# Optimization experiments

Measured on AMD Instinct MI355X. Metric: run time of the kernel, lower is better.

The kernel has to match this reference:

```python
import jax, jax.numpy as jnp
import numpy as np

LN_EPS = 1e-5


def _ln(h, g, b):
    mu = h.mean(-1, keepdims=True)
    var = ((h - mu) ** 2).mean(-1, keepdims=True)
    return (h - mu) / jnp.sqrt(var + LN_EPS) * g + b


def setup_inputs() -> dict:
    key = jax.random.key(0)
    ks = jax.random.split(key, 12)
    B, T, Cin, C, D, M = 16, 1024, 512, 1024, 256, 1024
    s = 0.02
    inp = {
        "x": jax.random.normal(ks[0], (B, T, Cin), jnp.float32),
        "masks": jnp.ones((B, T), jnp.float32),
        "W1": jax.random.normal(ks[1], (Cin, C), jnp.float32) * s,
        "g1": jnp.ones((C,), jnp.float32), "b1": jnp.zeros((C,), jnp.float32),
        "W2": jax.random.normal(ks[2], (C, C), jnp.float32) * s,
        "g2": jnp.ones((C,), jnp.float32), "b2": jnp.zeros((C,), jnp.float32),
        "W3": jax.random.normal(ks[3], (C, C), jnp.float32) * s,
        "g3": jnp.ones((C,), jnp.float32), "b3": jnp.zeros((C,), jnp.float32),
        "W4": jax.random.normal(ks[4], (C, C), jnp.float32) * s,
        "g4": jnp.ones((C,), jnp.float32), "b4": jnp.zeros((C,), jnp.float32),
        "W5": jax.random.normal(ks[5], (C, D), jnp.float32) * s,
        "b5": jnp.zeros((D,), jnp.float32),
        # Dirichlet(alpha=100) rows, as in the torch init: rows live on the simplex
        "embedding": jax.random.dirichlet(ks[6], jnp.full((D,), 100.0, jnp.float32), (M,)).astype(jnp.float32),
    }
    return inp


def reference(x, masks, W1, g1, b1, W2, g2, b2, W3, g3, b3, W4, g4, b4, W5, b5, embedding):
    h = jax.nn.relu(_ln(x @ W1, g1, b1))
    h = jax.nn.relu(_ln(h @ W2, g2, b2))
    h = jax.nn.relu(_ln(h @ W3, g3, b3))
    h = jax.nn.relu(_ln(h @ W4, g4, b4))
    z = h @ W5 + b5                              # [B, T, D]
    p = jax.nn.log_softmax(z, axis=-1)           # log-prob features

    B, T, D = p.shape
    p_flat = jax.lax.stop_gradient(p.reshape(-1, D))   # x.detach() in torch
    ep = jnp.exp(p_flat)                               # [N, D]
    # KL(exp(p) || e_m) summed over D, for all codes m:
    #   sum_d exp(p)*(p - log(e_m)) = rowsum(exp(p)*p) - exp(p) @ log(E)^T
    div = (ep * p_flat).sum(-1, keepdims=True) - ep @ jnp.log(embedding).T  # [N, M]
    idx = jnp.argmin(div, axis=-1)                     # [N]
    quant = jax.lax.stop_gradient(embedding[idx].reshape(B, T, D))

    # commitment loss: masked KL(exp(p) || quant.detach())
    kl = (jnp.exp(p) * (p - jnp.log(quant))).sum(-1)   # [B, T]
    loss = 0.25 * (kl * masks).mean(0).sum()

    # straight-through estimator
    q = p + jax.lax.stop_gradient(quant - p)
    return z, q, loss
```

## Files before the change

kernel.cpp:

```cpp
#include <hip/hip_runtime.h>
#include <hip/hip_bf16.h>
#include <stdint.h>

typedef __attribute__((ext_vector_type(4))) float f32x4;
typedef __attribute__((ext_vector_type(8))) __bf16 bf16x8;
typedef __attribute__((ext_vector_type(4))) __bf16 bf16x4;

#define LN_EPS 1e-5f

__device__ __forceinline__ void gload_lds16(const void* g, void* l) {
  __builtin_amdgcn_global_load_lds(
      (__attribute__((address_space(1))) void*)(uintptr_t)g,
      (__attribute__((address_space(3))) void*)(uint32_t)(uintptr_t)l,
      16, 0, 0);
}

__device__ __forceinline__ f32x4 mfma16(bf16x8 a, bf16x8 b, f32x4 c) {
  return __builtin_amdgcn_mfma_f32_16x16x32_bf16(a, b, c, 0, 0, 0);
}

__global__ __launch_bounds__(256) void k_cvt_bf16(const float* __restrict__ x,
                                                  __bf16* __restrict__ o) {
  int i = (blockIdx.x * 256 + threadIdx.x) * 8;
  f32x4 a = *(const f32x4*)(x + i);
  f32x4 b = *(const f32x4*)(x + i + 4);
  bf16x8 v;
#pragma unroll
  for (int j = 0; j < 4; ++j) { v[j] = (__bf16)a[j]; v[j + 4] = (__bf16)b[j]; }
  *(bf16x8*)(o + i) = v;
}

__global__ void k_transpose(const float* __restrict__ W, __bf16* __restrict__ Wt,
                            int K, int N) {
  __shared__ float t[32][33];
  int nt = blockIdx.x * 32, kt = blockIdx.y * 32;
  int tx = threadIdx.x, ty = threadIdx.y;
  t[ty][tx] = W[(size_t)(kt + ty) * N + nt + tx];
  __syncthreads();
  Wt[(size_t)(nt + ty) * K + kt + tx] = (__bf16)t[tx][ty];
}

__global__ void k_transpose3(const float* __restrict__ Wa, const float* __restrict__ Wb,
                             const float* __restrict__ Wc, __bf16* __restrict__ Ta,
                             __bf16* __restrict__ Tb, __bf16* __restrict__ Tc) {
  __shared__ float t[32][33];
  const float* W = blockIdx.z == 0 ? Wa : (blockIdx.z == 1 ? Wb : Wc);
  __bf16* T = blockIdx.z == 0 ? Ta : (blockIdx.z == 1 ? Tb : Tc);
  int nt = blockIdx.x * 32, kt = blockIdx.y * 32;
  int tx = threadIdx.x, ty = threadIdx.y;
  t[ty][tx] = W[(size_t)(kt + ty) * 1024 + nt + tx];
  __syncthreads();
  T[(size_t)(nt + ty) * 1024 + kt + tx] = (__bf16)t[tx][ty];
}

__global__ __launch_bounds__(256) void k_logE(const float* __restrict__ e,
                                              __bf16* __restrict__ o) {
  int i = blockIdx.x * 256 + threadIdx.x;
  o[i] = (__bf16)logf(e[i] * 256.0f);
}

__global__ __launch_bounds__(512, 2) void k_gemm256(
    const __bf16* __restrict__ A, const __bf16* __restrict__ Bt,
    __bf16* __restrict__ O, int N, int K) {
  __shared__ char lds[131072];
  const int tid = threadIdx.x;
  const int lane = tid & 63;
  const int wid = tid >> 6;
  const int wm = wid >> 2;
  const int wn = wid & 3;
  const int bm0 = blockIdx.x * 256;
  const int bn0 = blockIdx.y * 256;
  const int NT = K >> 6;

  const int slin = tid * 16;
  const int lrow = slin >> 7;
  const int scol = (slin & 127) ^ ((lrow & 7) << 4);
  const char* Ab = (const char*)A;
  const char* Bb = (const char*)Bt;
  const uint32_t rs = (uint32_t)K * 2;

  const int klo = (lane >> 4) * 16;
  const int sw = (lane & 7) << 4;
  const uint32_t kx0 = (uint32_t)(klo ^ sw);
  const uint32_t kx1 = (uint32_t)((64 + klo) ^ sw);
  const uint32_t abase = (uint32_t)(wm * 128 + (lane & 15)) * 128;
  const uint32_t bbase = (uint32_t)(wn * 64 + (lane & 15)) * 128;

  f32x4 acc[8][4];
#pragma unroll
  for (int i = 0; i < 8; ++i)
#pragma unroll
    for (int j = 0; j < 4; ++j) acc[i][j] = 0.0f;

#define LDSA(buf) (lds + (buf)*32768)
#define LDSB(buf) (lds + 65536 + (buf)*32768)
#define STAGE_A(t, h)                                                              \
  {                                                                                \
    const char* src = Ab + (size_t)(bm0 + (h)*128 + lrow) * rs + ((t) << 7) + scol;\
    char* dst = LDSA((t)&1) + (h)*16384 + slin;                                    \
    gload_lds16(src, dst);                                                         \
    gload_lds16(src + (size_t)64 * rs, dst + 8192);                                \
  }
#define STAGE_B(t, h)                                                              \
  {                                                                                \
    const char* src = Bb + (size_t)(bn0 + (h)*128 + lrow) * rs + ((t) << 7) + scol;\
    char* dst = LDSB((t)&1) + (h)*16384 + slin;                                    \
    gload_lds16(src, dst);                                                         \
    gload_lds16(src + (size_t)64 * rs, dst + 8192);                                \
  }

  STAGE_A(0, 0); STAGE_A(0, 1); STAGE_B(0, 0); STAGE_B(0, 1);
  STAGE_B(1, 0); STAGE_B(1, 1);
  asm volatile("s_waitcnt vmcnt(4)");
  __builtin_amdgcn_s_barrier();
  __builtin_amdgcn_sched_barrier(0);

  for (int t = 0; t < NT; ++t) {
    const char* Acur = LDSA(t & 1);
    const char* Bcur = LDSB(t & 1);

    if (t + 1 < NT) { STAGE_A(t + 1, 0); STAGE_A(t + 1, 1); }
    bf16x8 bF[4][2];
#pragma unroll
    for (int ni = 0; ni < 4; ++ni) {
      bF[ni][0] = *(const bf16x8*)(Bcur + bbase + ni * 2048 + kx0);
      bF[ni][1] = *(const bf16x8*)(Bcur + bbase + ni * 2048 + kx1);
    }
    {
      bf16x8 aF[4][2];
#pragma unroll
      for (int mi = 0; mi < 4; ++mi) {
        aF[mi][0] = *(const bf16x8*)(Acur + abase + mi * 2048 + kx0);
        aF[mi][1] = *(const bf16x8*)(Acur + abase + mi * 2048 + kx1);
      }
      __builtin_amdgcn_s_setprio(1);
#pragma unroll
      for (int mi = 0; mi < 4; ++mi)
#pragma unroll
        for (int ni = 0; ni < 4; ++ni) {
          acc[mi][ni] = mfma16(aF[mi][0], bF[ni][0], acc[mi][ni]);
          acc[mi][ni] = mfma16(aF[mi][1], bF[ni][1], acc[mi][ni]);
        }
      __builtin_amdgcn_s_setprio(0);
    }
    __builtin_amdgcn_s_barrier();
    __builtin_amdgcn_sched_barrier(0);

    if (t + 2 < NT) { STAGE_B(t + 2, 0); STAGE_B(t + 2, 1); }
    {
      bf16x8 aF[4][2];
#pragma unroll
      for (int mi = 0; mi < 4; ++mi) {
        aF[mi][0] = *(const bf16x8*)(Acur + abase + (mi + 4) * 2048 + kx0);
        aF[mi][1] = *(const bf16x8*)(Acur + abase + (mi + 4) * 2048 + kx1);
      }
      __builtin_amdgcn_s_setprio(1);
#pragma unroll
      for (int mi = 0; mi < 4; ++mi)
#pragma unroll
        for (int ni = 0; ni < 4; ++ni) {
          acc[mi + 4][ni] = mfma16(aF[mi][0], bF[ni][0], acc[mi + 4][ni]);
          acc[mi + 4][ni] = mfma16(aF[mi][1], bF[ni][1], acc[mi + 4][ni]);
        }
      __builtin_amdgcn_s_setprio(0);
    }
    if (t + 1 < NT) {
      asm volatile("s_waitcnt vmcnt(4)");
      __builtin_amdgcn_s_barrier();
      __builtin_amdgcn_sched_barrier(0);
    }
  }
#undef STAGE_A
#undef STAGE_B
#undef LDSA
#undef LDSB

  const int r0 = (lane >> 4) * 4;
  const int cc = lane & 15;
#pragma unroll
  for (int mi = 0; mi < 8; ++mi) {
#pragma unroll
    for (int ni = 0; ni < 4; ++ni) {
      int r = bm0 + wm * 128 + mi * 16 + r0;
      int c = bn0 + wn * 64 + ni * 16 + cc;
#pragma unroll
      for (int j = 0; j < 4; ++j)
        O[(size_t)(r + j) * N + c] = (__bf16)acc[mi][ni][j];
    }
  }
}

__global__ __launch_bounds__(256) void k_ln_relu(__bf16* __restrict__ h,
                                                 const float* __restrict__ g,
                                                 const float* __restrict__ b) {
  int lane = threadIdx.x & 63;
  int row = blockIdx.x * 4 + (threadIdx.x >> 6);
  __bf16* rp = h + (size_t)row * 1024;
  bf16x8 v0 = *(const bf16x8*)(rp + lane * 8);
  bf16x8 v1 = *(const bf16x8*)(rp + 512 + lane * 8);
  float f0[8], f1[8];
  float s = 0.f, sq = 0.f;
#pragma unroll
  for (int j = 0; j < 8; ++j) {
    f0[j] = (float)v0[j]; f1[j] = (float)v1[j];
    s += f0[j] + f1[j];
    sq += f0[j] * f0[j] + f1[j] * f1[j];
  }
#pragma unroll
  for (int d = 1; d < 64; d <<= 1) { s += __shfl_xor(s, d); sq += __shfl_xor(sq, d); }
  float mu = s * (1.0f / 1024.0f);
  float var = sq * (1.0f / 1024.0f) - mu * mu;
  float rstd = rsqrtf(var + LN_EPS);
  const f32x4* gv = (const f32x4*)g;
  const f32x4* bv = (const f32x4*)b;
  f32x4 ga0 = gv[lane * 2], ga1 = gv[lane * 2 + 1];
  f32x4 gb0 = gv[128 + lane * 2], gb1 = gv[128 + lane * 2 + 1];
  f32x4 ba0 = bv[lane * 2], ba1 = bv[lane * 2 + 1];
  f32x4 bb0 = bv[128 + lane * 2], bb1 = bv[128 + lane * 2 + 1];
  bf16x8 o0, o1;
#pragma unroll
  for (int j = 0; j < 4; ++j) {
    float t0 = (f0[j] - mu) * rstd * ga0[j] + ba0[j];
    float t1 = (f0[j + 4] - mu) * rstd * ga1[j] + ba1[j];
    float t2 = (f1[j] - mu) * rstd * gb0[j] + bb0[j];
    float t3 = (f1[j + 4] - mu) * rstd * gb1[j] + bb1[j];
    o0[j] = (__bf16)fmaxf(t0, 0.f);
    o0[j + 4] = (__bf16)fmaxf(t1, 0.f);
    o1[j] = (__bf16)fmaxf(t2, 0.f);
    o1[j + 4] = (__bf16)fmaxf(t3, 0.f);
  }
  *(bf16x8*)(rp + lane * 8) = o0;
  *(bf16x8*)(rp + 512 + lane * 8) = o1;
}

__global__ __launch_bounds__(256) void k_gemm_sm(
    const __bf16* __restrict__ A, const __bf16* __restrict__ Bt,
    const float* __restrict__ bias, float* __restrict__ z,
    __bf16* __restrict__ ep, float* __restrict__ sm) {
  const int K = 1024;
  __shared__ char lds[40960];
  char* ldsA = lds;
  char* ldsB = lds + 8192;
  const int tid = threadIdx.x;
  const int lane = tid & 63;
  const int wn = tid >> 6;
  const int bm0 = blockIdx.x * 64;
  const char* Ab = (const char*)A;
  const char* Bb = (const char*)Bt;
  const uint32_t rs = (uint32_t)K * 2;

  const int cc = lane & 15;
  uint32_t ra[2][4], rb[2][4];
  {
    const int sww = (lane & 7) << 4;
    const int gk = lane & 48;
#pragma unroll
    for (int kk = 0; kk < 2; ++kk) {
#pragma unroll
      for (int i = 0; i < 4; ++i) {
        uint32_t kb = (uint32_t)((kk * 64 + gk) ^ sww);
        ra[kk][i] = (uint32_t)(i * 16 + cc) * 128 + kb;
        rb[kk][i] = (uint32_t)(wn * 64 + i * 16 + cc) * 128 + kb;
      }
    }
  }

  f32x4 acc[4][4];
#pragma unroll
  for (int i = 0; i < 4; ++i)
#pragma unroll
    for (int j = 0; j < 4; ++j) acc[i][j] = 0.0f;

  for (int k0 = 0; k0 < K; k0 += 64) {
    __syncthreads();
#pragma unroll
    for (int i = 0; i < 2; ++i) {
      int lin = i * 4096 + tid * 16;
      int row = lin >> 7;
      int col = (lin & 127) ^ ((row & 7) << 4);
      gload_lds16(Ab + (size_t)(bm0 + row) * rs + k0 * 2 + col, ldsA + lin);
    }
#pragma unroll
    for (int i = 0; i < 8; ++i) {
      int lin = i * 4096 + tid * 16;
      int row = lin >> 7;
      int col = (lin & 127) ^ ((row & 7) << 4);
      gload_lds16(Bb + (size_t)row * rs + k0 * 2 + col, ldsB + lin);
    }
    __syncthreads();
#pragma unroll
    for (int kk = 0; kk < 2; ++kk) {
      bf16x8 af[4], bfv[4];
#pragma unroll
      for (int i = 0; i < 4; ++i) af[i] = *(const bf16x8*)(ldsA + ra[kk][i]);
#pragma unroll
      for (int i = 0; i < 4; ++i) bfv[i] = *(const bf16x8*)(ldsB + rb[kk][i]);
#pragma unroll
      for (int mi = 0; mi < 4; ++mi)
#pragma unroll
        for (int ni = 0; ni < 4; ++ni)
          acc[mi][ni] = mfma16(af[mi], bfv[ni], acc[mi][ni]);
    }
  }

  __syncthreads();
  float* stm = (float*)lds;
  float* sts = (float*)(lds + 1024);
  float* rowm = (float*)(lds + 2048);
  float* rows_ = (float*)(lds + 2304);

  const int r0 = (lane >> 4) * 4;
  float bvv[4];
#pragma unroll
  for (int ni = 0; ni < 4; ++ni) bvv[ni] = bias[wn * 64 + ni * 16 + cc];

#pragma unroll
  for (int mi = 0; mi < 4; ++mi) {
#pragma unroll
    for (int j = 0; j < 4; ++j) {
      float m = -3.4e38f;
#pragma unroll
      for (int ni = 0; ni < 4; ++ni) m = fmaxf(m, acc[mi][ni][j] + bvv[ni]);
#pragma unroll
      for (int d = 1; d < 16; d <<= 1) m = fmaxf(m, __shfl_xor(m, d));
      if (cc == 0) stm[wn * 64 + mi * 16 + r0 + j] = m;
    }
  }
  __syncthreads();
  if (tid < 64) {
    float m = fmaxf(fmaxf(stm[tid], stm[64 + tid]), fmaxf(stm[128 + tid], stm[192 + tid]));
    rowm[tid] = m;
  }
  __syncthreads();
#pragma unroll
  for (int mi = 0; mi < 4; ++mi) {
#pragma unroll
    for (int j = 0; j < 4; ++j) {
      int r = mi * 16 + r0 + j;
      float m = rowm[r];
      float s = 0.f;
#pragma unroll
      for (int ni = 0; ni < 4; ++ni) s += expf(acc[mi][ni][j] + bvv[ni] - m);
#pragma unroll
      for (int d = 1; d < 16; d <<= 1) s += __shfl_xor(s, d);
      if (cc == 0) sts[wn * 64 + r] = s;
    }
  }
  __syncthreads();
  if (tid < 64) {
    float s = sts[tid] + sts[64 + tid] + sts[128 + tid] + sts[192 + tid];
    rows_[tid] = s;
    sm[bm0 + tid] = rowm[tid] + logf(s);
  }
  __syncthreads();
#pragma unroll
  for (int mi = 0; mi < 4; ++mi) {
#pragma unroll
    for (int j = 0; j < 4; ++j) {
      int r = mi * 16 + r0 + j;
      float m = rowm[r];
      float inv = 1.0f / rows_[r];
      float* zp = z + (size_t)(bm0 + r) * 256;
      __bf16* epp = ep + (size_t)(bm0 + r) * 256;
#pragma unroll
      for (int ni = 0; ni < 4; ++ni) {
        int c = wn * 64 + ni * 16 + cc;
        float zz = acc[mi][ni][j] + bvv[ni];
        zp[c] = zz;
        epp[c] = (__bf16)(expf(zz - m) * inv);
      }
    }
  }
}

__global__ __launch_bounds__(256) void k_gemm_div(
    const __bf16* __restrict__ A, const __bf16* __restrict__ Bt,
    float* __restrict__ part_val, int* __restrict__ part_idx, int N, int K) {
  __shared__ char lds[32768];
  char* ldsA = lds;
  char* ldsB = lds + 16384;
  const int tid = threadIdx.x;
  const int lane = tid & 63;
  const int wid = tid >> 6;
  const int wm = wid >> 1, wn = wid & 1;
  const int bm0 = blockIdx.x * 128;
  const int bn0 = blockIdx.y * 128;

  const int slin = tid * 16;
  const int srow = slin >> 7;
  const int scol = (slin & 127) ^ ((srow & 7) << 4);

  const char* Ab = (const char*)A;
  const char* Bb = (const char*)Bt;
  const uint32_t rs = (uint32_t)K * 2;

  uint32_t ra[2][4], rb[2][4];
  {
    const int sw = (lane & 7) << 4;
    const int gk = lane & 48;
#pragma unroll
    for (int kk = 0; kk < 2; ++kk) {
#pragma unroll
      for (int i = 0; i < 4; ++i) {
        uint32_t kb = (uint32_t)((kk * 64 + gk) ^ sw);
        ra[kk][i] = (uint32_t)(wm * 64 + i * 16 + (lane & 15)) * 128 + kb;
        rb[kk][i] = (uint32_t)(wn * 64 + i * 16 + (lane & 15)) * 128 + kb;
      }
    }
  }

  f32x4 acc[4][4];
#pragma unroll
  for (int i = 0; i < 4; ++i)
#pragma unroll
    for (int j = 0; j < 4; ++j) acc[i][j] = 0.0f;

  for (int k0 = 0; k0 < K; k0 += 64) {
    __syncthreads();
    const uint32_t kbyte = (uint32_t)k0 * 2 + (uint32_t)scol;
#pragma unroll
    for (int i = 0; i < 4; ++i) {
      int row = i * 32 + srow;
      gload_lds16(Ab + (size_t)(bm0 + row) * rs + kbyte, ldsA + i * 4096 + slin);
    }
#pragma unroll
    for (int i = 0; i < 4; ++i) {
      int row = i * 32 + srow;
      gload_lds16(Bb + (size_t)(bn0 + row) * rs + kbyte, ldsB + i * 4096 + slin);
    }
    __syncthreads();
#pragma unroll
    for (int kk = 0; kk < 2; ++kk) {
      bf16x8 af[4], bfv[4];
#pragma unroll
      for (int i = 0; i < 4; ++i) af[i] = *(const bf16x8*)(ldsA + ra[kk][i]);
#pragma unroll
      for (int i = 0; i < 4; ++i) bfv[i] = *(const bf16x8*)(ldsB + rb[kk][i]);
#pragma unroll
      for (int mi = 0; mi < 4; ++mi)
#pragma unroll
        for (int ni = 0; ni < 4; ++ni)
          acc[mi][ni] = mfma16(af[mi], bfv[ni], acc[mi][ni]);
    }
  }

  const int r0 = (lane >> 4) * 4;
  const int cc = lane & 15;
  const int nch = N >> 6;
#pragma unroll
  for (int mi = 0; mi < 4; ++mi) {
#pragma unroll
    for (int j = 0; j < 4; ++j) {
      float v = acc[mi][0][j];
      int c = cc;
#pragma unroll
      for (int ni = 1; ni < 4; ++ni) {
        float v2 = acc[mi][ni][j];
        int c2 = ni * 16 + cc;
        if (v2 > v) { v = v2; c = c2; }
      }
#pragma unroll
      for (int d = 1; d < 16; d <<= 1) {
        float ov = __shfl_xor(v, d);
        int oc = __shfl_xor(c, d);
        if (ov > v || (ov == v && oc < c)) { v = ov; c = oc; }
      }
      if (cc == 0) {
        int r = bm0 + wm * 64 + mi * 16 + r0 + j;
        int chunk = (bn0 >> 6) + wn;
        part_val[r * nch + chunk] = v;
        part_idx[r * nch + chunk] = bn0 + wn * 64 + c;
      }
    }
  }
}

__global__ __launch_bounds__(256) void k_final(
    const float* __restrict__ part_val, const int* __restrict__ part_idx,
    const float* __restrict__ z, const float* __restrict__ sm,
    const float* __restrict__ emb, const float* __restrict__ masks,
    float* __restrict__ q, float* __restrict__ blockloss) {
  __shared__ float ls[4];
  int lane = threadIdx.x & 63;
  int w = threadIdx.x >> 6;
  int row = blockIdx.x * 4 + w;
  float v = -3.4e38f;
  int c = 0x7fffffff;
  if (lane < 16) { v = part_val[row * 16 + lane]; c = part_idx[row * 16 + lane]; }
#pragma unroll
  for (int d = 1; d < 16; d <<= 1) {
    float ov = __shfl_xor(v, d);
    int oc = __shfl_xor(c, d);
    if (ov > v || (ov == v && oc < c)) { v = ov; c = oc; }
  }
  int code = __shfl(c, 0);
  f32x4 ev = ((const f32x4*)(emb + (size_t)code * 256))[lane];
  ((f32x4*)(q + (size_t)row * 256))[lane] = ev;
  f32x4 zv = ((const f32x4*)(z + (size_t)row * 256))[lane];
  float smr = sm[row];
  float kl = 0.f;
#pragma unroll
  for (int j = 0; j < 4; ++j) {
    float pj = zv[j] - smr;
    kl += expf(pj) * (pj - logf(ev[j]));
  }
#pragma unroll
  for (int d = 1; d < 64; d <<= 1) kl += __shfl_xor(kl, d);
  if (lane == 0) ls[w] = kl * masks[row];
  __syncthreads();
  if (threadIdx.x == 0) blockloss[blockIdx.x] = ls[0] + ls[1] + ls[2] + ls[3];
}

__global__ __launch_bounds__(256) void k_loss_reduce(const float* __restrict__ bl,
                                                     float* __restrict__ out) {
  __shared__ float s[256];
  float a = 0.f;
#pragma unroll
  for (int i = 0; i < 16; ++i) a += bl[threadIdx.x + i * 256];
  s[threadIdx.x] = a;
  __syncthreads();
  for (int st = 128; st > 0; st >>= 1) {
    if (threadIdx.x < st) s[threadIdx.x] += s[threadIdx.x + st];
    __syncthreads();
  }
  if (threadIdx.x == 0) out[0] = s[0] * (0.25f / 16.0f);
}

extern "C" void kernel_launch(void* const* d_in, const int* in_sizes, int n_in,
                              void* d_out, int out_size, void* d_ws, size_t ws_size,
                              hipStream_t stream) {
  const float* x = (const float*)d_in[0];
  const float* masks = (const float*)d_in[1];
  const float* W1 = (const float*)d_in[2];
  const float* g1 = (const float*)d_in[3];
  const float* b1 = (const float*)d_in[4];
  const float* W2 = (const float*)d_in[5];
  const float* g2 = (const float*)d_in[6];
  const float* b2 = (const float*)d_in[7];
  const float* W3 = (const float*)d_in[8];
  const float* g3 = (const float*)d_in[9];
  const float* b3 = (const float*)d_in[10];
  const float* W4 = (const float*)d_in[11];
  const float* g4 = (const float*)d_in[12];
  const float* b4 = (const float*)d_in[13];
  const float* W5 = (const float*)d_in[14];
  const float* b5 = (const float*)d_in[15];
  const float* emb = (const float*)d_in[16];

  const int M = 16384;
  char* ws = (char*)d_ws;
  __bf16* bufA = (__bf16*)(ws);
  __bf16* bufB = (__bf16*)(ws + (32ull << 20));
  __bf16* W1t = (__bf16*)(ws + (64ull << 20));
  __bf16* W2t = (__bf16*)(ws + (65ull << 20));
  __bf16* W3t = (__bf16*)(ws + (67ull << 20));
  __bf16* W4t = (__bf16*)(ws + (69ull << 20));
  __bf16* W5t = (__bf16*)(ws + (71ull << 20));
  __bf16* logE = (__bf16*)(ws + (72ull << 20));
  float* part_val = (float*)(ws + (73ull << 20));
  int* part_idx = (int*)(ws + (74ull << 20));
  float* blockloss = (float*)(ws + (75ull << 20));
  float* sm = (float*)(ws + (76ull << 20));
  __bf16* ep = (__bf16*)(ws + (16ull << 20));

  float* z = (float*)d_out;
  float* q = z + (size_t)M * 256;
  float* lossp = z + 2ull * M * 256;

  dim3 tb32(32, 32);
  k_cvt_bf16<<<4096, 256, 0, stream>>>(x, bufB);
  k_transpose<<<dim3(32, 16), tb32, 0, stream>>>(W1, W1t, 512, 1024);
  k_transpose3<<<dim3(32, 32, 3), tb32, 0, stream>>>(W2, W3, W4, W2t, W3t, W4t);
  k_transpose<<<dim3(8, 32), tb32, 0, stream>>>(W5, W5t, 1024, 256);
  k_logE<<<1024, 256, 0, stream>>>(emb, logE);

  k_gemm256<<<dim3(64, 4), 512, 0, stream>>>(bufB, W1t, bufA, 1024, 512);
  k_ln_relu<<<4096, 256, 0, stream>>>(bufA, g1, b1);
  k_gemm256<<<dim3(64, 4), 512, 0, stream>>>(bufA, W2t, bufB, 1024, 1024);
  k_ln_relu<<<4096, 256, 0, stream>>>(bufB, g2, b2);
  k_gemm256<<<dim3(64, 4), 512, 0, stream>>>(bufB, W3t, bufA, 1024, 1024);
  k_ln_relu<<<4096, 256, 0, stream>>>(bufA, g3, b3);
  k_gemm256<<<dim3(64, 4), 512, 0, stream>>>(bufA, W4t, bufB, 1024, 1024);
  k_ln_relu<<<4096, 256, 0, stream>>>(bufB, g4, b4);
  k_gemm_sm<<<256, 256, 0, stream>>>(bufB, W5t, b5, z, ep, sm);
  k_gemm_div<<<dim3(128, 8), 256, 0, stream>>>(ep, logE, part_val, part_idx, 1024, 256);
  k_final<<<4096, 256, 0, stream>>>(part_val, part_idx, z, sm, emb, masks, q, blockloss);
  k_loss_reduce<<<1, 256, 0, stream>>>(blockloss, lossp);
}
```

Baseline: 271.0 us.

## Fuse LayerNorm+ReLU into GEMM epilogue stats and next GEMM's A-load prologue

Removes the four standalone LayerNorm+ReLU kernels. Each GEMM epilogue now writes per-row partial sums and sums of squares for its column block. The next GEMM (or the final small GEMM) turns these into mean and rstd, then normalizes, scales, shifts and applies ReLU to its A tiles as they pass through registers before being written to swizzled LDS. This saves a full read and write pass over the 16K x 1024 activation per layer, plus the extra launches. In exchange, A staging moves from direct global-to-LDS loads to register loads with ALU work inside the pipelined loop. Variance now comes from fp32 sums of squares over the unrounded accumulators.

Measured after the change: 265.5 us. 2.0% less time.

```diff
diff --git a/kernel.cpp b/kernel.cpp
--- a/kernel.cpp
+++ b/kernel.cpp
@@ -3,6 +3,7 @@
 #include <stdint.h>
 
 typedef __attribute__((ext_vector_type(4))) float f32x4;
+typedef __attribute__((ext_vector_type(2))) float f32x2;
 typedef __attribute__((ext_vector_type(8))) __bf16 bf16x8;
 typedef __attribute__((ext_vector_type(4))) __bf16 bf16x4;
 
@@ -59,10 +60,14 @@
   o[i] = (__bf16)logf(e[i] * 256.0f);
 }
 
+template <int MODE>
 __global__ __launch_bounds__(512, 2) void k_gemm256(
     const __bf16* __restrict__ A, const __bf16* __restrict__ Bt,
-    __bf16* __restrict__ O, int N, int K) {
-  __shared__ char lds[131072];
+    __bf16* __restrict__ O, const float* __restrict__ gw,
+    const float* __restrict__ bw, const f32x2* __restrict__ inPart,
+    f32x2* __restrict__ outPart, int N, int K) {
+  __shared__ char lds[139264];
+  const int GB = 131072;
   const int tid = threadIdx.x;
   const int lane = tid & 63;
   const int wid = tid >> 6;
@@ -86,6 +91,12 @@
   const uint32_t abase = (uint32_t)(wm * 128 + (lane & 15)) * 128;
   const uint32_t bbase = (uint32_t)(wn * 64 + (lane & 15)) * 128;
 
+  const int alrow = tid >> 3;
+  const uint32_t acolb = (uint32_t)(tid & 7) * 16;
+  const uint32_t awcol = acolb ^ (uint32_t)((alrow & 7) << 4);
+  float aS[4], cS[4];
+  bf16x8 ar[4];
+
   f32x4 acc[8][4];
 #pragma unroll
   for (int i = 0; i < 8; ++i)
@@ -108,18 +119,80 @@
     gload_lds16(src, dst);                                                         \
     gload_lds16(src + (size_t)64 * rs, dst + 8192);                                \
   }
-
-  STAGE_A(0, 0); STAGE_A(0, 1); STAGE_B(0, 0); STAGE_B(0, 1);
-  STAGE_B(1, 0); STAGE_B(1, 1);
-  asm volatile("s_waitcnt vmcnt(4)");
-  __builtin_amdgcn_s_barrier();
-  __builtin_amdgcn_sched_barrier(0);
+#define A_ISSUE(t1)                                                                \
+  {                                                                                \
+    const char* base_ = Ab + (size_t)(bm0 + alrow) * rs + ((size_t)(t1) << 7) + acolb; \
+    ar[0] = *(const bf16x8*)(base_);                                               \
+    ar[1] = *(const bf16x8*)(base_ + (size_t)64 * rs);                             \
+    ar[2] = *(const bf16x8*)(base_ + (size_t)128 * rs);                            \
+    ar[3] = *(const bf16x8*)(base_ + (size_t)192 * rs);                            \
+  }
+#define A_WRITE(t1)                                                                \
+  {                                                                                \
+    uint32_t gb_ = GB + (uint32_t)(t1)*256 + (uint32_t)(tid & 7) * 32;             \
+    f32x4 g0 = *(const f32x4*)(lds + gb_), g1 = *(const f32x4*)(lds + gb_ + 16);   \
+    f32x4 b0 = *(const f32x4*)(lds + gb_ + 4096), b1 = *(const f32x4*)(lds + gb_ + 4112); \
+    char* wb_ = LDSA((t1)&1);                                                      \
+    _Pragma("unroll") for (int i = 0; i < 4; ++i) {                                \
+      bf16x8 v = ar[i], o;                                                         \
+      _Pragma("unroll") for (int e = 0; e < 8; ++e) {                              \
+        float xv = (float)v[e];                                                    \
+        float tt = fmaf(xv, aS[i], cS[i]);                                         \
+        float ge = e < 4 ? g0[e] : g1[e - 4];                                      \
+        float be = e < 4 ? b0[e] : b1[e - 4];                                      \
+        tt = fmaf(tt, ge, be);                                                     \
+        o[e] = (__bf16)fmaxf(tt, 0.f);                                             \
+      }                                                                            \
+      *(bf16x8*)(wb_ + (i >> 1) * 16384 + (alrow + (i & 1) * 64) * 128 + awcol) = o; \
+    }                                                                              \
+  }
+
+  if constexpr (MODE == 1) {
+    if (tid < 256) {
+      ((f32x4*)(lds + GB))[tid] = ((const f32x4*)gw)[tid];
+      ((f32x4*)(lds + GB + 4096))[tid] = ((const f32x4*)bw)[tid];
+    }
+#pragma unroll
+    for (int i = 0; i < 4; ++i) {
+      int r = bm0 + (i >> 1) * 128 + (i & 1) * 64 + alrow;
+      const f32x4* pp = (const f32x4*)(inPart + (size_t)r * 4);
+      f32x4 p0 = pp[0], p1 = pp[1];
+      float s = p0[0] + p0[2] + p1[0] + p1[2];
+      float q = p0[1] + p0[3] + p1[1] + p1[3];
+      float mu = s * (1.0f / 1024.0f);
+      float var = q * (1.0f / 1024.0f) - mu * mu;
+      float rstd = rsqrtf(var + LN_EPS);
+      aS[i] = rstd;
+      cS[i] = -mu * rstd;
+    }
+    __builtin_amdgcn_sched_barrier(0);
+    A_ISSUE(0)
+    STAGE_B(0, 0); STAGE_B(0, 1); STAGE_B(1, 0); STAGE_B(1, 1);
+    __builtin_amdgcn_sched_barrier(0);
+    asm volatile("s_waitcnt lgkmcnt(0)");
+    __builtin_amdgcn_s_barrier();
+    asm volatile("s_waitcnt vmcnt(8)");
+    A_WRITE(0)
+    asm volatile("s_waitcnt vmcnt(4) lgkmcnt(0)");
+    __builtin_amdgcn_s_barrier();
+    __builtin_amdgcn_sched_barrier(0);
+  } else {
+    STAGE_A(0, 0); STAGE_A(0, 1); STAGE_B(0, 0); STAGE_B(0, 1);
+    STAGE_B(1, 0); STAGE_B(1, 1);
+    asm volatile("s_waitcnt vmcnt(4)");
+    __builtin_amdgcn_s_barrier();
+    __builtin_amdgcn_sched_barrier(0);
+  }
 
   for (int t = 0; t < NT; ++t) {
     const char* Acur = LDSA(t & 1);
     const char* Bcur = LDSB(t & 1);
 
-    if (t + 1 < NT) { STAGE_A(t + 1, 0); STAGE_A(t + 1, 1); }
+    if (t + 1 < NT) {
+      if constexpr (MODE == 1) { A_ISSUE(t + 1) }
+      else { STAGE_A(t + 1, 0); STAGE_A(t + 1, 1); }
+    }
+    __builtin_amdgcn_sched_barrier(0);
     bf16x8 bF[4][2];
 #pragma unroll
     for (int ni = 0; ni < 4; ++ni) {
@@ -147,6 +220,7 @@
     __builtin_amdgcn_sched_barrier(0);
 
     if (t + 2 < NT) { STAGE_B(t + 2, 0); STAGE_B(t + 2, 1); }
+    __builtin_amdgcn_sched_barrier(0);
     {
       bf16x8 aF[4][2];
 #pragma unroll
@@ -165,18 +239,56 @@
       __builtin_amdgcn_s_setprio(0);
     }
     if (t + 1 < NT) {
-      asm volatile("s_waitcnt vmcnt(4)");
+      if (t + 2 < NT) { asm volatile("s_waitcnt vmcnt(4)"); }
+      else            { asm volatile("s_waitcnt vmcnt(0)"); }
+      if constexpr (MODE == 1) {
+        A_WRITE(t + 1)
+        asm volatile("s_waitcnt lgkmcnt(0)");
+      }
       __builtin_amdgcn_s_barrier();
       __builtin_amdgcn_sched_barrier(0);
     }
   }
 #undef STAGE_A
 #undef STAGE_B
+#undef A_ISSUE
+#undef A_WRITE
 #undef LDSA
 #undef LDSB
 
   const int r0 = (lane >> 4) * 4;
   const int cc = lane & 15;
+
+  __builtin_amdgcn_s_barrier();
+  float* stp = (float*)lds;
+  float* stq = (float*)(lds + 4096);
+#pragma unroll
+  for (int mi = 0; mi < 8; ++mi) {
+#pragma unroll
+    for (int j = 0; j < 4; ++j) {
+      float s = 0.f, q = 0.f;
+#pragma unroll
+      for (int ni = 0; ni < 4; ++ni) {
+        float v = acc[mi][ni][j];
+        s += v; q += v * v;
+      }
+#pragma unroll
+      for (int d = 1; d < 16; d <<= 1) { s += __shfl_xor(s, d); q += __shfl_xor(q, d); }
+      if (cc == 0) {
+        int rl = wm * 128 + mi * 16 + r0 + j;
+        stp[rl * 4 + wn] = s;
+        stq[rl * 4 + wn] = q;
+      }
+    }
+  }
+  __syncthreads();
+  if (tid < 256) {
+    float s = stp[tid * 4] + stp[tid * 4 + 1] + stp[tid * 4 + 2] + stp[tid * 4 + 3];
+    float q = stq[tid * 4] + stq[tid * 4 + 1] + stq[tid * 4 + 2] + stq[tid * 4 + 3];
+    f32x2 pr; pr[0] = s; pr[1] = q;
+    outPart[(size_t)(bm0 + tid) * 4 + blockIdx.y] = pr;
+  }
+
 #pragma unroll
   for (int mi = 0; mi < 8; ++mi) {
 #pragma unroll
@@ -190,55 +302,14 @@
   }
 }
 
-__global__ __launch_bounds__(256) void k_ln_relu(__bf16* __restrict__ h,
-                                                 const float* __restrict__ g,
-                                                 const float* __restrict__ b) {
-  int lane = threadIdx.x & 63;
-  int row = blockIdx.x * 4 + (threadIdx.x >> 6);
-  __bf16* rp = h + (size_t)row * 1024;
-  bf16x8 v0 = *(const bf16x8*)(rp + lane * 8);
-  bf16x8 v1 = *(const bf16x8*)(rp + 512 + lane * 8);
-  float f0[8], f1[8];
-  float s = 0.f, sq = 0.f;
-#pragma unroll
-  for (int j = 0; j < 8; ++j) {
-    f0[j] = (float)v0[j]; f1[j] = (float)v1[j];
-    s += f0[j] + f1[j];
-    sq += f0[j] * f0[j] + f1[j] * f1[j];
-  }
-#pragma unroll
-  for (int d = 1; d < 64; d <<= 1) { s += __shfl_xor(s, d); sq += __shfl_xor(sq, d); }
-  float mu = s * (1.0f / 1024.0f);
-  float var = sq * (1.0f / 1024.0f) - mu * mu;
-  float rstd = rsqrtf(var + LN_EPS);
-  const f32x4* gv = (const f32x4*)g;
-  const f32x4* bv = (const f32x4*)b;
-  f32x4 ga0 = gv[lane * 2], ga1 = gv[lane * 2 + 1];
-  f32x4 gb0 = gv[128 + lane * 2], gb1 = gv[128 + lane * 2 + 1];
-  f32x4 ba0 = bv[lane * 2], ba1 = bv[lane * 2 + 1];
-  f32x4 bb0 = bv[128 + lane * 2], bb1 = bv[128 + lane * 2 + 1];
-  bf16x8 o0, o1;
-#pragma unroll
-  for (int j = 0; j < 4; ++j) {
-    float t0 = (f0[j] - mu) * rstd * ga0[j] + ba0[j];
-    float t1 = (f0[j + 4] - mu) * rstd * ga1[j] + ba1[j];
-    float t2 = (f1[j] - mu) * rstd * gb0[j] + bb0[j];
-    float t3 = (f1[j + 4] - mu) * rstd * gb1[j] + bb1[j];
-    o0[j] = (__bf16)fmaxf(t0, 0.f);
-    o0[j + 4] = (__bf16)fmaxf(t1, 0.f);
-    o1[j] = (__bf16)fmaxf(t2, 0.f);
-    o1[j + 4] = (__bf16)fmaxf(t3, 0.f);
-  }
-  *(bf16x8*)(rp + lane * 8) = o0;
-  *(bf16x8*)(rp + 512 + lane * 8) = o1;
-}
-
 __global__ __launch_bounds__(256) void k_gemm_sm(
     const __bf16* __restrict__ A, const __bf16* __restrict__ Bt,
-    const float* __restrict__ bias, float* __restrict__ z,
-    __bf16* __restrict__ ep, float* __restrict__ sm) {
+    const float* __restrict__ gw, const float* __restrict__ bw,
+    const f32x2* __restrict__ inPart, const float* __restrict__ bias,
+    float* __restrict__ z, __bf16* __restrict__ ep, float* __restrict__ sm) {
   const int K = 1024;
-  __shared__ char lds[40960];
+  __shared__ char lds[49152];
+  const int GBS = 40960;
   char* ldsA = lds;
   char* ldsB = lds + 8192;
   const int tid = threadIdx.x;
@@ -248,8 +319,28 @@
   const char* Ab = (const char*)A;
   const char* Bb = (const char*)Bt;
   const uint32_t rs = (uint32_t)K * 2;
-
   const int cc = lane & 15;
+
+  ((f32x4*)(lds + GBS))[tid] = ((const f32x4*)gw)[tid];
+  ((f32x4*)(lds + GBS + 4096))[tid] = ((const f32x4*)bw)[tid];
+
+  const int ar0 = tid >> 3;
+  float aS[2], cS[2];
+#pragma unroll
+  for (int i = 0; i < 2; ++i) {
+    int r = bm0 + ar0 + i * 32;
+    const f32x4* pp = (const f32x4*)(inPart + (size_t)r * 4);
+    f32x4 p0 = pp[0], p1 = pp[1];
+    float s = p0[0] + p0[2] + p1[0] + p1[2];
+    float q = p0[1] + p0[3] + p1[1] + p1[3];
+    float mu = s * (1.0f / 1024.0f);
+    float var = q * (1.0f / 1024.0f) - mu * mu;
+    float rstd = rsqrtf(var + LN_EPS);
+    aS[i] = rstd; cS[i] = -mu * rstd;
+  }
+  const uint32_t acolb = (uint32_t)(tid & 7) * 16;
+  const uint32_t awcol = acolb ^ (uint32_t)((ar0 & 7) << 4);
+
   uint32_t ra[2][4], rb[2][4];
   {
     const int sww = (lane & 7) << 4;
@@ -273,19 +364,35 @@
 
   for (int k0 = 0; k0 < K; k0 += 64) {
     __syncthreads();
-#pragma unroll
-    for (int i = 0; i < 2; ++i) {
-      int lin = i * 4096 + tid * 16;
-      int row = lin >> 7;
-      int col = (lin & 127) ^ ((row & 7) << 4);
-      gload_lds16(Ab + (size_t)(bm0 + row) * rs + k0 * 2 + col, ldsA + lin);
-    }
+    const char* abase_ = Ab + (size_t)(bm0 + ar0) * rs + (size_t)k0 * 2 + acolb;
+    bf16x8 a0 = *(const bf16x8*)abase_;
+    bf16x8 a1 = *(const bf16x8*)(abase_ + (size_t)32 * rs);
+    __builtin_amdgcn_sched_barrier(0);
 #pragma unroll
     for (int i = 0; i < 8; ++i) {
       int lin = i * 4096 + tid * 16;
       int row = lin >> 7;
       int col = (lin & 127) ^ ((row & 7) << 4);
       gload_lds16(Bb + (size_t)row * rs + k0 * 2 + col, ldsB + lin);
+    }
+    __builtin_amdgcn_sched_barrier(0);
+    asm volatile("s_waitcnt vmcnt(8)");
+    {
+      uint32_t gb_ = GBS + (uint32_t)k0 * 4 + (uint32_t)(tid & 7) * 32;
+      f32x4 g0 = *(const f32x4*)(lds + gb_), g1 = *(const f32x4*)(lds + gb_ + 16);
+      f32x4 b0 = *(const f32x4*)(lds + gb_ + 4096), b1 = *(const f32x4*)(lds + gb_ + 4112);
+      bf16x8 o0, o1;
+#pragma unroll
+      for (int e = 0; e < 8; ++e) {
+        float ge = e < 4 ? g0[e] : g1[e - 4];
+        float be = e < 4 ? b0[e] : b1[e - 4];
+        float t0 = fmaf(fmaf((float)a0[e], aS[0], cS[0]), ge, be);
+        float t1 = fmaf(fmaf((float)a1[e], aS[1], cS[1]), ge, be);
+        o0[e] = (__bf16)fmaxf(t0, 0.f);
+        o1[e] = (__bf16)fmaxf(t1, 0.f);
+      }
+      *(bf16x8*)(ldsA + ar0 * 128 + awcol) = o0;
+      *(bf16x8*)(ldsA + (ar0 + 32) * 128 + awcol) = o1;
     }
     __syncthreads();
 #pragma unroll
@@ -561,6 +668,8 @@
   int* part_idx = (int*)(ws + (74ull << 20));
   float* blockloss = (float*)(ws + (75ull << 20));
   float* sm = (float*)(ws + (76ull << 20));
+  f32x2* partA = (f32x2*)(ws + (77ull << 20));
+  f32x2* partB = (f32x2*)(ws + (78ull << 20));
   __bf16* ep = (__bf16*)(ws + (16ull << 20));
 
   float* z = (float*)d_out;
@@ -574,15 +683,15 @@
   k_transpose<<<dim3(8, 32), tb32, 0, stream>>>(W5, W5t, 1024, 256);
   k_logE<<<1024, 256, 0, stream>>>(emb, logE);
 
-  k_gemm256<<<dim3(64, 4), 512, 0, stream>>>(bufB, W1t, bufA, 1024, 512);
-  k_ln_relu<<<4096, 256, 0, stream>>>(bufA, g1, b1);
-  k_gemm256<<<dim3(64, 4), 512, 0, stream>>>(bufA, W2t, bufB, 1024, 1024);
-  k_ln_relu<<<4096, 256, 0, stream>>>(bufB, g2, b2);
-  k_gemm256<<<dim3(64, 4), 512, 0, stream>>>(bufB, W3t, bufA, 1024, 1024);
-  k_ln_relu<<<4096, 256, 0, stream>>>(bufA, g3, b3);
-  k_gemm256<<<dim3(64, 4), 512, 0, stream>>>(bufA, W4t, bufB, 1024, 1024);
-  k_ln_relu<<<4096, 256, 0, stream>>>(bufB, g4, b4);
-  k_gemm_sm<<<256, 256, 0, stream>>>(bufB, W5t, b5, z, ep, sm);
+  k_gemm256<0><<<dim3(64, 4), 512, 0, stream>>>(bufB, W1t, bufA, nullptr, nullptr,
+                                                nullptr, partA, 1024, 512);
+  k_gemm256<1><<<dim3(64, 4), 512, 0, stream>>>(bufA, W2t, bufB, g1, b1,
+                                                partA, partB, 1024, 1024);
+  k_gemm256<1><<<dim3(64, 4), 512, 0, stream>>>(bufB, W3t, bufA, g2, b2,
+                                                partB, partA, 1024, 1024);
+  k_gemm256<1><<<dim3(64, 4), 512, 0, stream>>>(bufA, W4t, bufB, g3, b3,
+                                                partA, partB, 1024, 1024);
+  k_gemm_sm<<<256, 256, 0, stream>>>(bufB, W5t, g4, b4, partB, b5, z, ep, sm);
   k_gemm_div<<<dim3(128, 8), 256, 0, stream>>>(ep, logE, part_val, part_idx, 1024, 256);
   k_final<<<4096, 256, 0, stream>>>(part_val, part_idx, z, sm, emb, masks, q, blockloss);
   k_loss_reduce<<<1, 256, 0, stream>>>(blockloss, lossp);
```

## Fuse last LayerNorm stats into GEMM epilogue and apply LN in W5 GEMM prologue

Applied to the files above, without the earlier changes.

The big GEMM is restructured into an 8-phase schedule with finer barrier and waitcnt interleaving of staging loads and MFMA work. Its 4th-layer variant also emits per-row partial sum and sum-of-squares. The W5 GEMM now loads raw activations through registers and applies LayerNorm plus ReLU while writing them to LDS. This removes one standalone LN kernel launch and its full read/write pass over the activation. The tradeoff is more barriers per K-step, variance computed as E[x^2]-mu^2 on fp32 accumulators before bf16 rounding, and A loads in the small GEMM no longer going straight to LDS.

New measurement: 264.1 us. 1.03x faster.

```diff
diff --git a/kernel.cpp b/kernel.cpp
--- a/kernel.cpp
+++ b/kernel.cpp
@@ -3,6 +3,7 @@
 #include <stdint.h>
 
 typedef __attribute__((ext_vector_type(4))) float f32x4;
+typedef __attribute__((ext_vector_type(2))) float f32x2;
 typedef __attribute__((ext_vector_type(8))) __bf16 bf16x8;
 typedef __attribute__((ext_vector_type(4))) __bf16 bf16x4;
 
@@ -59,9 +60,10 @@
   o[i] = (__bf16)logf(e[i] * 256.0f);
 }
 
-__global__ __launch_bounds__(512, 2) void k_gemm256(
+template <int STATS>
+__global__ __launch_bounds__(512, 2) void k_gemm8p(
     const __bf16* __restrict__ A, const __bf16* __restrict__ Bt,
-    __bf16* __restrict__ O, int N, int K) {
+    __bf16* __restrict__ O, f32x2* __restrict__ outPart, int N, int K) {
   __shared__ char lds[131072];
   const int tid = threadIdx.x;
   const int lane = tid & 63;
@@ -71,6 +73,7 @@
   const int bm0 = blockIdx.x * 256;
   const int bn0 = blockIdx.y * 256;
   const int NT = K >> 6;
+  const int NI = NT >> 1;
 
   const int slin = tid * 16;
   const int lrow = slin >> 7;
@@ -91,6 +94,7 @@
   for (int i = 0; i < 8; ++i)
 #pragma unroll
     for (int j = 0; j < 4; ++j) acc[i][j] = 0.0f;
+  bf16x8 bF[4][2];
 
 #define LDSA(buf) (lds + (buf)*32768)
 #define LDSB(buf) (lds + 65536 + (buf)*32768)
@@ -108,75 +112,118 @@
     gload_lds16(src, dst);                                                         \
     gload_lds16(src + (size_t)64 * rs, dst + 8192);                                \
   }
-
-  STAGE_A(0, 0); STAGE_A(0, 1); STAGE_B(0, 0); STAGE_B(0, 1);
-  STAGE_B(1, 0); STAGE_B(1, 1);
+#define NOSTG {}
+#define VM4 asm volatile("s_waitcnt vmcnt(4)");
+#define VM0 asm volatile("s_waitcnt vmcnt(0)");
+#define VMN
+#define PH(q, Ac, Bc, DOB, STG, VM)                                                \
+  {                                                                                \
+    bf16x8 a0k0 = *(const bf16x8*)((Ac) + abase + (2 * (q)) * 2048 + kx0);         \
+    bf16x8 a0k1 = *(const bf16x8*)((Ac) + abase + (2 * (q)) * 2048 + kx1);         \
+    bf16x8 a1k0 = *(const bf16x8*)((Ac) + abase + (2 * (q) + 1) * 2048 + kx0);     \
+    bf16x8 a1k1 = *(const bf16x8*)((Ac) + abase + (2 * (q) + 1) * 2048 + kx1);     \
+    if (DOB) {                                                                     \
+      _Pragma("unroll") for (int ni = 0; ni < 4; ++ni) {                           \
+        bF[ni][0] = *(const bf16x8*)((Bc) + bbase + ni * 2048 + kx0);              \
+        bF[ni][1] = *(const bf16x8*)((Bc) + bbase + ni * 2048 + kx1);              \
+      }                                                                            \
+    }                                                                              \
+    STG                                                                            \
+    __builtin_amdgcn_s_barrier();                                                  \
+    asm volatile("s_waitcnt lgkmcnt(0)");                                          \
+    __builtin_amdgcn_sched_barrier(0);                                             \
+    __builtin_amdgcn_s_setprio(1);                                                 \
+    _Pragma("unroll") for (int ni = 0; ni < 4; ++ni) {                             \
+      acc[2 * (q)][ni] = mfma16(a0k0, bF[ni][0], acc[2 * (q)][ni]);                \
+      acc[2 * (q)][ni] = mfma16(a0k1, bF[ni][1], acc[2 * (q)][ni]);                \
+      acc[2 * (q) + 1][ni] = mfma16(a1k0, bF[ni][0], acc[2 * (q) + 1][ni]);        \
+      acc[2 * (q) + 1][ni] = mfma16(a1k1, bF[ni][1], acc[2 * (q) + 1][ni]);        \
+    }                                                                              \
+    __builtin_amdgcn_s_setprio(0);                                                 \
+    VM                                                                             \
+    __builtin_amdgcn_s_barrier();                                                  \
+    __builtin_amdgcn_sched_barrier(0);                                             \
+  }
+
+  STAGE_A(0, 0) STAGE_A(0, 1) STAGE_B(0, 0) STAGE_B(0, 1)
+  STAGE_B(1, 0) STAGE_B(1, 1)
   asm volatile("s_waitcnt vmcnt(4)");
   __builtin_amdgcn_s_barrier();
   __builtin_amdgcn_sched_barrier(0);
 
-  for (int t = 0; t < NT; ++t) {
-    const char* Acur = LDSA(t & 1);
-    const char* Bcur = LDSB(t & 1);
-
-    if (t + 1 < NT) { STAGE_A(t + 1, 0); STAGE_A(t + 1, 1); }
-    bf16x8 bF[4][2];
-#pragma unroll
-    for (int ni = 0; ni < 4; ++ni) {
-      bF[ni][0] = *(const bf16x8*)(Bcur + bbase + ni * 2048 + kx0);
-      bF[ni][1] = *(const bf16x8*)(Bcur + bbase + ni * 2048 + kx1);
-    }
-    {
-      bf16x8 aF[4][2];
-#pragma unroll
-      for (int mi = 0; mi < 4; ++mi) {
-        aF[mi][0] = *(const bf16x8*)(Acur + abase + mi * 2048 + kx0);
-        aF[mi][1] = *(const bf16x8*)(Acur + abase + mi * 2048 + kx1);
-      }
-      __builtin_amdgcn_s_setprio(1);
-#pragma unroll
-      for (int mi = 0; mi < 4; ++mi)
-#pragma unroll
-        for (int ni = 0; ni < 4; ++ni) {
-          acc[mi][ni] = mfma16(aF[mi][0], bF[ni][0], acc[mi][ni]);
-          acc[mi][ni] = mfma16(aF[mi][1], bF[ni][1], acc[mi][ni]);
-        }
-      __builtin_amdgcn_s_setprio(0);
-    }
-    __builtin_amdgcn_s_barrier();
-    __builtin_amdgcn_sched_barrier(0);
-
-    if (t + 2 < NT) { STAGE_B(t + 2, 0); STAGE_B(t + 2, 1); }
-    {
-      bf16x8 aF[4][2];
-#pragma unroll
-      for (int mi = 0; mi < 4; ++mi) {
-        aF[mi][0] = *(const bf16x8*)(Acur + abase + (mi + 4) * 2048 + kx0);
-        aF[mi][1] = *(const bf16x8*)(Acur + abase + (mi + 4) * 2048 + kx1);
-      }
-      __builtin_amdgcn_s_setprio(1);
-#pragma unroll
-      for (int mi = 0; mi < 4; ++mi)
-#pragma unroll
-        for (int ni = 0; ni < 4; ++ni) {
-          acc[mi + 4][ni] = mfma16(aF[mi][0], bF[ni][0], acc[mi + 4][ni]);
-          acc[mi + 4][ni] = mfma16(aF[mi][1], bF[ni][1], acc[mi + 4][ni]);
-        }
-      __builtin_amdgcn_s_setprio(0);
-    }
-    if (t + 1 < NT) {
-      asm volatile("s_waitcnt vmcnt(4)");
-      __builtin_amdgcn_s_barrier();
-      __builtin_amdgcn_sched_barrier(0);
-    }
-  }
+  const char* A0c = LDSA(0);
+  const char* B0c = LDSB(0);
+  const char* A1c = LDSA(1);
+  const char* B1c = LDSB(1);
+
+  for (int J = 0; J < NI - 1; ++J) {
+    const int t0 = 2 * J;
+    const int t1 = t0 + 1;
+    PH(0, A0c, B0c, 1, STAGE_A(t1, 0), VMN)
+    PH(1, A0c, B0c, 0, STAGE_A(t1, 1), VMN)
+    PH(2, A0c, B0c, 0, STAGE_B(t0 + 2, 0), VMN)
+    PH(3, A0c, B0c, 0, STAGE_B(t0 + 2, 1), VM4)
+    PH(0, A1c, B1c, 1, STAGE_A(t0 + 2, 0), VMN)
+    PH(1, A1c, B1c, 0, STAGE_A(t0 + 2, 1), VMN)
+    PH(2, A1c, B1c, 0, STAGE_B(t1 + 2, 0), VMN)
+    PH(3, A1c, B1c, 0, STAGE_B(t1 + 2, 1), VM4)
+  }
+  {
+    const int t1 = NT - 1;
+    PH(0, A0c, B0c, 1, STAGE_A(t1, 0), VMN)
+    PH(1, A0c, B0c, 0, STAGE_A(t1, 1), VMN)
+    PH(2, A0c, B0c, 0, NOSTG, VMN)
+    PH(3, A0c, B0c, 0, NOSTG, VM0)
+    PH(0, A1c, B1c, 1, NOSTG, VMN)
+    PH(1, A1c, B1c, 0, NOSTG, VMN)
+    PH(2, A1c, B1c, 0, NOSTG, VMN)
+    PH(3, A1c, B1c, 0, NOSTG, VMN)
+  }
+#undef PH
 #undef STAGE_A
 #undef STAGE_B
 #undef LDSA
 #undef LDSB
+#undef NOSTG
+#undef VM4
+#undef VM0
+#undef VMN
 
   const int r0 = (lane >> 4) * 4;
   const int cc = lane & 15;
+
+  if constexpr (STATS == 1) {
+    __builtin_amdgcn_s_barrier();
+    float* stp = (float*)lds;
+    float* stq = (float*)(lds + 4096);
+#pragma unroll
+    for (int mi = 0; mi < 8; ++mi) {
+#pragma unroll
+      for (int j = 0; j < 4; ++j) {
+        float s = 0.f, q = 0.f;
+#pragma unroll
+        for (int ni = 0; ni < 4; ++ni) {
+          float v = acc[mi][ni][j];
+          s += v; q += v * v;
+        }
+#pragma unroll
+        for (int d = 1; d < 16; d <<= 1) { s += __shfl_xor(s, d); q += __shfl_xor(q, d); }
+        if (cc == 0) {
+          int rl = wm * 128 + mi * 16 + r0 + j;
+          stp[rl * 4 + wn] = s;
+          stq[rl * 4 + wn] = q;
+        }
+      }
+    }
+    __syncthreads();
+    if (tid < 256) {
+      float s = stp[tid * 4] + stp[tid * 4 + 1] + stp[tid * 4 + 2] + stp[tid * 4 + 3];
+      float q = stq[tid * 4] + stq[tid * 4 + 1] + stq[tid * 4 + 2] + stq[tid * 4 + 3];
+      f32x2 pr; pr[0] = s; pr[1] = q;
+      outPart[(size_t)(bm0 + tid) * 4 + blockIdx.y] = pr;
+    }
+  }
+
 #pragma unroll
   for (int mi = 0; mi < 8; ++mi) {
 #pragma unroll
@@ -235,10 +282,12 @@
 
 __global__ __launch_bounds__(256) void k_gemm_sm(
     const __bf16* __restrict__ A, const __bf16* __restrict__ Bt,
-    const float* __restrict__ bias, float* __restrict__ z,
-    __bf16* __restrict__ ep, float* __restrict__ sm) {
+    const float* __restrict__ gw, const float* __restrict__ bw,
+    const f32x2* __restrict__ inPart, const float* __restrict__ bias,
+    float* __restrict__ z, __bf16* __restrict__ ep, float* __restrict__ sm) {
   const int K = 1024;
-  __shared__ char lds[40960];
+  __shared__ char lds[49152];
+  const int GBS = 40960;
   char* ldsA = lds;
   char* ldsB = lds + 8192;
   const int tid = threadIdx.x;
@@ -248,8 +297,28 @@
   const char* Ab = (const char*)A;
   const char* Bb = (const char*)Bt;
   const uint32_t rs = (uint32_t)K * 2;
-
   const int cc = lane & 15;
+
+  ((f32x4*)(lds + GBS))[tid] = ((const f32x4*)gw)[tid];
+  ((f32x4*)(lds + GBS + 4096))[tid] = ((const f32x4*)bw)[tid];
+
+  const int ar0 = tid >> 3;
+  float aS[2], cS[2];
+#pragma unroll
+  for (int i = 0; i < 2; ++i) {
+    int r = bm0 + ar0 + i * 32;
+    const f32x4* pp = (const f32x4*)(inPart + (size_t)r * 4);
+    f32x4 p0 = pp[0], p1 = pp[1];
+    float s = p0[0] + p0[2] + p1[0] + p1[2];
+    float q = p0[1] + p0[3] + p1[1] + p1[3];
+    float mu = s * (1.0f / 1024.0f);
+    float var = q * (1.0f / 1024.0f) - mu * mu;
+    float rstd = rsqrtf(var + LN_EPS);
+    aS[i] = rstd; cS[i] = -mu * rstd;
+  }
+  const uint32_t acolb = (uint32_t)(tid & 7) * 16;
+  const uint32_t awcol = acolb ^ (uint32_t)((ar0 & 7) << 4);
+
   uint32_t ra[2][4], rb[2][4];
   {
     const int sww = (lane & 7) << 4;
@@ -273,19 +342,35 @@
 
   for (int k0 = 0; k0 < K; k0 += 64) {
     __syncthreads();
-#pragma unroll
-    for (int i = 0; i < 2; ++i) {
-      int lin = i * 4096 + tid * 16;
-      int row = lin >> 7;
-      int col = (lin & 127) ^ ((row & 7) << 4);
-      gload_lds16(Ab + (size_t)(bm0 + row) * rs + k0 * 2 + col, ldsA + lin);
-    }
+    const char* abase_ = Ab + (size_t)(bm0 + ar0) * rs + (size_t)k0 * 2 + acolb;
+    bf16x8 a0 = *(const bf16x8*)abase_;
+    bf16x8 a1 = *(const bf16x8*)(abase_ + (size_t)32 * rs);
+    __builtin_amdgcn_sched_barrier(0);
 #pragma unroll
     for (int i = 0; i < 8; ++i) {
       int lin = i * 4096 + tid * 16;
       int row = lin >> 7;
       int col = (lin & 127) ^ ((row & 7) << 4);
       gload_lds16(Bb + (size_t)row * rs + k0 * 2 + col, ldsB + lin);
+    }
+    __builtin_amdgcn_sched_barrier(0);
+    asm volatile("s_waitcnt vmcnt(8)");
+    {
+      uint32_t gb_ = GBS + (uint32_t)k0 * 4 + (uint32_t)(tid & 7) * 32;
+      f32x4 g0 = *(const f32x4*)(lds + gb_), g1 = *(const f32x4*)(lds + gb_ + 16);
+      f32x4 b0 = *(const f32x4*)(lds + gb_ + 4096), b1 = *(const f32x4*)(lds + gb_ + 4112);
+      bf16x8 o0, o1;
+#pragma unroll
+      for (int e = 0; e < 8; ++e) {
+        float ge = e < 4 ? g0[e] : g1[e - 4];
+        float be = e < 4 ? b0[e] : b1[e - 4];
+        float t0 = fmaf(fmaf((float)a0[e], aS[0], cS[0]), ge, be);
+        float t1 = fmaf(fmaf((float)a1[e], aS[1], cS[1]), ge, be);
+        o0[e] = (__bf16)fmaxf(t0, 0.f);
+        o1[e] = (__bf16)fmaxf(t1, 0.f);
+      }
+      *(bf16x8*)(ldsA + ar0 * 128 + awcol) = o0;
+      *(bf16x8*)(ldsA + (ar0 + 32) * 128 + awcol) = o1;
     }
     __syncthreads();
 #pragma unroll
@@ -561,6 +646,7 @@
   int* part_idx = (int*)(ws + (74ull << 20));
   float* blockloss = (float*)(ws + (75ull << 20));
   float* sm = (float*)(ws + (76ull << 20));
+  f32x2* partB = (f32x2*)(ws + (78ull << 20));
   __bf16* ep = (__bf16*)(ws + (16ull << 20));
 
   float* z = (float*)d_out;
@@ -574,15 +660,14 @@
   k_transpose<<<dim3(8, 32), tb32, 0, stream>>>(W5, W5t, 1024, 256);
   k_logE<<<1024, 256, 0, stream>>>(emb, logE);
 
-  k_gemm256<<<dim3(64, 4), 512, 0, stream>>>(bufB, W1t, bufA, 1024, 512);
+  k_gemm8p<0><<<dim3(64, 4), 512, 0, stream>>>(bufB, W1t, bufA, nullptr, 1024, 512);
   k_ln_relu<<<4096, 256, 0, stream>>>(bufA, g1, b1);
-  k_gemm256<<<dim3(64, 4), 512, 0, stream>>>(bufA, W2t, bufB, 1024, 1024);
+  k_gemm8p<0><<<dim3(64, 4), 512, 0, stream>>>(bufA, W2t, bufB, nullptr, 1024, 1024);
   k_ln_relu<<<4096, 256, 0, stream>>>(bufB, g2, b2);
-  k_gemm256<<<dim3(64, 4), 512, 0, stream>>>(bufB, W3t, bufA, 1024, 1024);
+  k_gemm8p<0><<<dim3(64, 4), 512, 0, stream>>>(bufB, W3t, bufA, nullptr, 1024, 1024);
   k_ln_relu<<<4096, 256, 0, stream>>>(bufA, g3, b3);
-  k_gemm256<<<dim3(64, 4), 512, 0, stream>>>(bufA, W4t, bufB, 1024, 1024);
-  k_ln_relu<<<4096, 256, 0, stream>>>(bufB, g4, b4);
-  k_gemm_sm<<<256, 256, 0, stream>>>(bufB, W5t, b5, z, ep, sm);
+  k_gemm8p<1><<<dim3(64, 4), 512, 0, stream>>>(bufA, W4t, bufB, partB, 1024, 1024);
+  k_gemm_sm<<<256, 256, 0, stream>>>(bufB, W5t, g4, b4, partB, b5, z, ep, sm);
   k_gemm_div<<<dim3(128, 8), 256, 0, stream>>>(ep, logE, part_val, part_idx, 1024, 256);
   k_final<<<4096, 256, 0, stream>>>(part_val, part_idx, z, sm, emb, masks, q, blockloss);
   k_loss_reduce<<<1, 256, 0, stream>>>(blockloss, lossp);
```
